# Kernel tuning notes

Measured on AMD Instinct MI355X. Metric: run time of the kernel, lower is better.

The kernel has to match this reference:

```python
import jax, jax.numpy as jnp
import numpy as np

EPS = 1e-12  # torch F.normalize eps

def _l2norm(v, axis):
    n = jnp.sqrt(jnp.sum(v * v, axis=axis, keepdims=True))
    return v / jnp.maximum(n, EPS)

def setup_inputs() -> dict:
    key = jax.random.key(0)
    k1, k2 = jax.random.split(key)
    B, N, D, K = 8, 2048, 128, 64
    x = jax.random.normal(k1, (B, N, D), dtype=jnp.float32)
    std1 = 1.0 / np.sqrt(K * D)
    centroids = jax.random.uniform(k2, (K, D), dtype=jnp.float32, minval=-std1, maxval=std1)
    return {"x": x, "centroids": centroids}

def reference(x, centroids):
    # x: [B, N, D], centroids: [K, D]
    B, N, D = x.shape
    K = centroids.shape[0]
    xn = _l2norm(x, axis=-1)                       # descriptor-wise L2 normalize
    res = xn[:, :, None, :] - centroids[None, None]  # [B, N, K, D]
    dist = jnp.sum(res * res, axis=-1)             # [B, N, K] squared distances
    assign = jax.nn.softmax(dist, axis=-1)         # softmax over clusters (NOTE: positive distances, as in source)
    vlad = jnp.einsum('bnk,bnkd->bkd', assign, res)  # weighted residual sum over N
    vlad = _l2norm(vlad, axis=2)                   # intra-normalization per cluster
    vlad = vlad.reshape(B, K * D)
    vlad = _l2norm(vlad, axis=1)                   # global L2 normalize
    return vlad
```

## Files before the change

### kernel.cpp

```cpp
#include <hip/hip_runtime.h>
#include <math.h>

#define BB 8
#define NN 2048
#define DD 128
#define KK 64
#define PP 128
#define NPB (NN / PP)

__global__ __launch_bounds__(256)
__attribute__((amdgpu_waves_per_eu(4, 4)))
void netvlad_k1(
    const float* __restrict__ x, const float* __restrict__ cent,
    float* __restrict__ part_acc)
{
    const int b    = blockIdx.x >> 7;
    const int p    = blockIdx.x & 127;
    const int t    = threadIdx.x;
    const int kq   = t >> 3;
    const int pr   = t & 7;
    const int dbase = pr * 16;
    const int wave = t >> 6;

    __shared__ __align__(16) float xs[NPB][DD];
    __shared__ __align__(16) float sL[NPB][4];

    int off[4];
    #pragma unroll
    for (int jj = 0; jj < 4; ++jj) off[jj] = dbase + (((jj + pr) & 3) << 2);

    const int i0 = t >> 4, tl = t & 15;
    const float* xr = x + ((size_t)b * NN + (size_t)p * NPB + i0) * DD;
    float4 v0 = *(const float4*)(xr + tl * 4);
    float4 v1 = *(const float4*)(xr + 64 + tl * 4);

    float4 cA[4], cB[4];
    float cn2a = 0.f, cn2b = 0.f;
    #pragma unroll
    for (int jj = 0; jj < 4; ++jj) {
        cA[jj] = *(const float4*)(cent + (2 * kq) * DD + off[jj]);
        cB[jj] = *(const float4*)(cent + (2 * kq + 1) * DD + off[jj]);
        cn2a += cA[jj].x*cA[jj].x + cA[jj].y*cA[jj].y + cA[jj].z*cA[jj].z + cA[jj].w*cA[jj].w;
        cn2b += cB[jj].x*cB[jj].x + cB[jj].y*cB[jj].y + cB[jj].z*cB[jj].z + cB[jj].w*cB[jj].w;
    }
    #pragma unroll
    for (int m = 1; m < 8; m <<= 1) {
        cn2a += __shfl_xor(cn2a, m);
        cn2b += __shfl_xor(cn2b, m);
    }

    {
        float ss = v0.x*v0.x + v0.y*v0.y + v0.z*v0.z + v0.w*v0.w
                 + v1.x*v1.x + v1.y*v1.y + v1.z*v1.z + v1.w*v1.w;
        #pragma unroll
        for (int m = 1; m < 16; m <<= 1) ss += __shfl_xor(ss, m);
        const float rn = 1.0f / fmaxf(sqrtf(ss), 1e-12f);
        v0.x *= rn; v0.y *= rn; v0.z *= rn; v0.w *= rn;
        v1.x *= rn; v1.y *= rn; v1.z *= rn; v1.w *= rn;
        *(float4*)(&xs[i0][tl * 4])      = v0;
        *(float4*)(&xs[i0][64 + tl * 4]) = v1;
    }
    __syncthreads();

    float e0[NPB], e1[NPB];
    #pragma unroll
    for (int i = 0; i < NPB; ++i) {
        float S0 = 0.f, S1 = 0.f;
        #pragma unroll
        for (int jj = 0; jj < 4; ++jj) {
            float4 v = *(const float4*)(&xs[i][off[jj]]);
            S0 += v.x*cA[jj].x + v.y*cA[jj].y + v.z*cA[jj].z + v.w*cA[jj].w;
            S1 += v.x*cB[jj].x + v.y*cB[jj].y + v.z*cB[jj].z + v.w*cB[jj].w;
        }
        #pragma unroll
        for (int m = 1; m < 8; m <<= 1) {
            S0 += __shfl_xor(S0, m);
            S1 += __shfl_xor(S1, m);
        }
        e0[i] = __expf(cn2a - 2.f * S0);
        e1[i] = __expf(cn2b - 2.f * S1);
        float es = e0[i] + e1[i];
        #pragma unroll
        for (int m = 8; m < 64; m <<= 1) es += __shfl_xor(es, m);
        if ((t & 63) == 0) sL[i][wave] = es;
    }
    __syncthreads();

    float4 acc0[4], acc1[4];
    #pragma unroll
    for (int jj = 0; jj < 4; ++jj) {
        acc0[jj] = make_float4(0.f, 0.f, 0.f, 0.f);
        acc1[jj] = make_float4(0.f, 0.f, 0.f, 0.f);
    }
    float sA0 = 0.f, sA1 = 0.f;
    #pragma unroll
    for (int i = 0; i < NPB; ++i) {
        const float4 s4 = *(const float4*)(&sL[i][0]);
        const float rs = 1.0f / (s4.x + s4.y + s4.z + s4.w);
        const float a0 = e0[i] * rs, a1 = e1[i] * rs;
        sA0 += a0; sA1 += a1;
        #pragma unroll
        for (int jj = 0; jj < 4; ++jj) {
            float4 v = *(const float4*)(&xs[i][off[jj]]);
            acc0[jj].x += a0*v.x; acc0[jj].y += a0*v.y; acc0[jj].z += a0*v.z; acc0[jj].w += a0*v.w;
            acc1[jj].x += a1*v.x; acc1[jj].y += a1*v.y; acc1[jj].z += a1*v.z; acc1[jj].w += a1*v.w;
        }
    }

    const size_t base = (size_t)(b * PP + p) * KK * DD;
    #pragma unroll
    for (int jj = 0; jj < 4; ++jj) {
        const float4 c0 = *(const float4*)(cent + (2 * kq) * DD + off[jj]);
        const float4 c1 = *(const float4*)(cent + (2 * kq + 1) * DD + off[jj]);
        acc0[jj].x -= sA0 * c0.x; acc0[jj].y -= sA0 * c0.y;
        acc0[jj].z -= sA0 * c0.z; acc0[jj].w -= sA0 * c0.w;
        acc1[jj].x -= sA1 * c1.x; acc1[jj].y -= sA1 * c1.y;
        acc1[jj].z -= sA1 * c1.z; acc1[jj].w -= sA1 * c1.w;
        *(float4*)(part_acc + base + (2 * kq) * DD + off[jj])     = acc0[jj];
        *(float4*)(part_acc + base + (2 * kq + 1) * DD + off[jj]) = acc1[jj];
    }
}

__global__ __launch_bounds__(512) void netvlad_k2(
    const float* __restrict__ part_acc, float* __restrict__ out)
{
    const int b  = blockIdx.x >> 6;
    const int k  = blockIdx.x & 63;
    const int t  = threadIdx.x;
    const int d4 = t & 31;
    const int ps = t >> 5;

    float4 acc = make_float4(0.f, 0.f, 0.f, 0.f);
    const float* base = part_acc + ((size_t)(b * PP) * KK + k) * DD + d4 * 4;
    #pragma unroll
    for (int j = 0; j < 8; ++j) {
        const float4 v = *(const float4*)(base + (size_t)(j * 16 + ps) * KK * DD);
        acc.x += v.x; acc.y += v.y; acc.z += v.z; acc.w += v.w;
    }

    __shared__ __align__(16) float4 red[16][32];
    red[ps][d4] = acc;
    __syncthreads();

    if (t < 32) {
        float4 v = red[0][t];
        #pragma unroll
        for (int s = 1; s < 16; ++s) {
            v.x += red[s][t].x; v.y += red[s][t].y;
            v.z += red[s][t].z; v.w += red[s][t].w;
        }
        float ss = v.x*v.x + v.y*v.y + v.z*v.z + v.w*v.w;
        #pragma unroll
        for (int m = 1; m < 32; m <<= 1) ss += __shfl_xor(ss, m);
        const float rn = 0.125f / fmaxf(sqrtf(ss), 1e-12f);
        v.x *= rn; v.y *= rn; v.z *= rn; v.w *= rn;
        *(float4*)(out + ((size_t)b * KK + k) * DD + t * 4) = v;
    }
}

extern "C" void kernel_launch(void* const* d_in, const int* in_sizes, int n_in,
                              void* d_out, int out_size, void* d_ws, size_t ws_size,
                              hipStream_t stream) {
    const float* x    = (const float*)d_in[0];
    const float* cent = (const float*)d_in[1];
    float* out = (float*)d_out;

    float* part_acc = (float*)d_ws;

    netvlad_k1<<<dim3(BB * PP), dim3(256), 0, stream>>>(x, cent, part_acc);
    netvlad_k2<<<dim3(BB * KK), dim3(512), 0, stream>>>(part_acc, out);
}
```

Before: 96.64 us.

## Split k1 block into two halves and combine partials in shared memory

Kernel 1 now uses 512 threads per block. Two groups of 256 threads each process 16 points, and their accumulators are summed through shared memory before the block writes its result. The number of point-chunks drops from 128 to 64, which halves the partial-accumulator buffer written to global memory and read back by kernel 2. The costs are an extra shared-memory reduction, a barrier, higher LDS use, and half as many blocks in kernel 1.

```diff
diff --git a/kernel.cpp b/kernel.cpp
--- a/kernel.cpp
+++ b/kernel.cpp
@@ -5,32 +5,37 @@
 #define NN 2048
 #define DD 128
 #define KK 64
-#define PP 128
+#define PP 64
 #define NPB (NN / PP)
+#define TI 16
 
-__global__ __launch_bounds__(256)
+__global__ __launch_bounds__(512)
 __attribute__((amdgpu_waves_per_eu(4, 4)))
 void netvlad_k1(
     const float* __restrict__ x, const float* __restrict__ cent,
     float* __restrict__ part_acc)
 {
-    const int b    = blockIdx.x >> 7;
-    const int p    = blockIdx.x & 127;
+    const int b    = blockIdx.x >> 6;
+    const int p    = blockIdx.x & 63;
     const int t    = threadIdx.x;
-    const int kq   = t >> 3;
-    const int pr   = t & 7;
+    const int h    = t >> 8;
+    const int u    = t & 255;
+    const int kq   = u >> 3;
+    const int pr   = u & 7;
     const int dbase = pr * 16;
-    const int wave = t >> 6;
+    const int wv   = u >> 6;
 
-    __shared__ __align__(16) float xs[NPB][DD];
-    __shared__ __align__(16) float sL[NPB][4];
+    __shared__ __align__(16) float xs[2][TI][DD];
+    __shared__ __align__(16) float sL[2][TI][4];
+    __shared__ __align__(16) float comb[256][36];
+    __shared__ float sAc[32][2];
 
     int off[4];
     #pragma unroll
     for (int jj = 0; jj < 4; ++jj) off[jj] = dbase + (((jj + pr) & 3) << 2);
 
-    const int i0 = t >> 4, tl = t & 15;
-    const float* xr = x + ((size_t)b * NN + (size_t)p * NPB + i0) * DD;
+    const int i0 = u >> 4, tl = u & 15;
+    const float* xr = x + ((size_t)b * NN + (size_t)p * NPB + h * TI + i0) * DD;
     float4 v0 = *(const float4*)(xr + tl * 4);
     float4 v1 = *(const float4*)(xr + 64 + tl * 4);
 
@@ -57,18 +62,18 @@
         const float rn = 1.0f / fmaxf(sqrtf(ss), 1e-12f);
         v0.x *= rn; v0.y *= rn; v0.z *= rn; v0.w *= rn;
         v1.x *= rn; v1.y *= rn; v1.z *= rn; v1.w *= rn;
-        *(float4*)(&xs[i0][tl * 4])      = v0;
-        *(float4*)(&xs[i0][64 + tl * 4]) = v1;
+        *(float4*)(&xs[h][i0][tl * 4])      = v0;
+        *(float4*)(&xs[h][i0][64 + tl * 4]) = v1;
     }
     __syncthreads();
 
-    float e0[NPB], e1[NPB];
+    float e0[TI], e1[TI];
     #pragma unroll
-    for (int i = 0; i < NPB; ++i) {
+    for (int i = 0; i < TI; ++i) {
         float S0 = 0.f, S1 = 0.f;
         #pragma unroll
         for (int jj = 0; jj < 4; ++jj) {
-            float4 v = *(const float4*)(&xs[i][off[jj]]);
+            float4 v = *(const float4*)(&xs[h][i][off[jj]]);
             S0 += v.x*cA[jj].x + v.y*cA[jj].y + v.z*cA[jj].z + v.w*cA[jj].w;
             S1 += v.x*cB[jj].x + v.y*cB[jj].y + v.z*cB[jj].z + v.w*cB[jj].w;
         }
@@ -82,7 +87,7 @@
         float es = e0[i] + e1[i];
         #pragma unroll
         for (int m = 8; m < 64; m <<= 1) es += __shfl_xor(es, m);
-        if ((t & 63) == 0) sL[i][wave] = es;
+        if ((u & 63) == 0) sL[h][i][wv] = es;
     }
     __syncthreads();
 
@@ -94,30 +99,47 @@
     }
     float sA0 = 0.f, sA1 = 0.f;
     #pragma unroll
-    for (int i = 0; i < NPB; ++i) {
-        const float4 s4 = *(const float4*)(&sL[i][0]);
+    for (int i = 0; i < TI; ++i) {
+        const float4 s4 = *(const float4*)(&sL[h][i][0]);
         const float rs = 1.0f / (s4.x + s4.y + s4.z + s4.w);
         const float a0 = e0[i] * rs, a1 = e1[i] * rs;
         sA0 += a0; sA1 += a1;
         #pragma unroll
         for (int jj = 0; jj < 4; ++jj) {
-            float4 v = *(const float4*)(&xs[i][off[jj]]);
+            float4 v = *(const float4*)(&xs[h][i][off[jj]]);
             acc0[jj].x += a0*v.x; acc0[jj].y += a0*v.y; acc0[jj].z += a0*v.z; acc0[jj].w += a0*v.w;
             acc1[jj].x += a1*v.x; acc1[jj].y += a1*v.y; acc1[jj].z += a1*v.z; acc1[jj].w += a1*v.w;
         }
     }
 
-    const size_t base = (size_t)(b * PP + p) * KK * DD;
-    #pragma unroll
-    for (int jj = 0; jj < 4; ++jj) {
-        const float4 c0 = *(const float4*)(cent + (2 * kq) * DD + off[jj]);
-        const float4 c1 = *(const float4*)(cent + (2 * kq + 1) * DD + off[jj]);
-        acc0[jj].x -= sA0 * c0.x; acc0[jj].y -= sA0 * c0.y;
-        acc0[jj].z -= sA0 * c0.z; acc0[jj].w -= sA0 * c0.w;
-        acc1[jj].x -= sA1 * c1.x; acc1[jj].y -= sA1 * c1.y;
-        acc1[jj].z -= sA1 * c1.z; acc1[jj].w -= sA1 * c1.w;
-        *(float4*)(part_acc + base + (2 * kq) * DD + off[jj])     = acc0[jj];
-        *(float4*)(part_acc + base + (2 * kq + 1) * DD + off[jj]) = acc1[jj];
+    if (h == 0) {
+        #pragma unroll
+        for (int jj = 0; jj < 4; ++jj) {
+            *(float4*)(&comb[u][jj * 4])      = acc0[jj];
+            *(float4*)(&comb[u][16 + jj * 4]) = acc1[jj];
+        }
+        if (pr == 0) { sAc[kq][0] = sA0; sAc[kq][1] = sA1; }
+    }
+    __syncthreads();
+
+    if (h == 1) {
+        sA0 += sAc[kq][0];
+        sA1 += sAc[kq][1];
+        const size_t base = (size_t)(b * PP + p) * KK * DD;
+        #pragma unroll
+        for (int jj = 0; jj < 4; ++jj) {
+            const float4 o0 = *(const float4*)(&comb[u][jj * 4]);
+            const float4 o1 = *(const float4*)(&comb[u][16 + jj * 4]);
+            float4 r0 = acc0[jj], r1 = acc1[jj];
+            r0.x += o0.x; r0.y += o0.y; r0.z += o0.z; r0.w += o0.w;
+            r1.x += o1.x; r1.y += o1.y; r1.z += o1.z; r1.w += o1.w;
+            r0.x -= sA0 * cA[jj].x; r0.y -= sA0 * cA[jj].y;
+            r0.z -= sA0 * cA[jj].z; r0.w -= sA0 * cA[jj].w;
+            r1.x -= sA1 * cB[jj].x; r1.y -= sA1 * cB[jj].y;
+            r1.z -= sA1 * cB[jj].z; r1.w -= sA1 * cB[jj].w;
+            *(float4*)(part_acc + base + (2 * kq) * DD + off[jj])     = r0;
+            *(float4*)(part_acc + base + (2 * kq + 1) * DD + off[jj]) = r1;
+        }
     }
 }
 
@@ -133,7 +155,7 @@
     float4 acc = make_float4(0.f, 0.f, 0.f, 0.f);
     const float* base = part_acc + ((size_t)(b * PP) * KK + k) * DD + d4 * 4;
     #pragma unroll
-    for (int j = 0; j < 8; ++j) {
+    for (int j = 0; j < 4; ++j) {
         const float4 v = *(const float4*)(base + (size_t)(j * 16 + ps) * KK * DD);
         acc.x += v.x; acc.y += v.y; acc.z += v.z; acc.w += v.w;
     }
@@ -167,6 +189,6 @@
 
     float* part_acc = (float*)d_ws;
 
-    netvlad_k1<<<dim3(BB * PP), dim3(256), 0, stream>>>(x, cent, part_acc);
+    netvlad_k1<<<dim3(BB * PP), dim3(512), 0, stream>>>(x, cent, part_acc);
     netvlad_k2<<<dim3(BB * KK), dim3(512), 0, stream>>>(part_acc, out);
 }
```

Result: faster. 92.82 us (-3.9%).
